# Optimization experiments

Hardware: AMD Instinct MI355X
Metric: run time of the kernel (lower is better)

The kernel has to match this reference:

```python
import jax, jax.numpy as jnp
import numpy as np
from jax import lax

COND, PRED, DH, NOUT = 64, 32, 128, 1
M, LQ, N, LR = 8, 256, 64, 512


def setup_inputs() -> dict:
    key = jax.random.key(0)
    ks = jax.random.split(key, 8)
    g = lambda k, sh, s=0.05: jax.random.normal(k, sh, jnp.float32) * s
    return {
        "query": jax.random.normal(ks[0], (M, LQ), jnp.float32),
        "ref": jax.random.normal(ks[1], (N, LR), jnp.float32),
        "q_weight": g(ks[2], (DH, 1, COND)),
        "q_bias": jnp.zeros((DH,), jnp.float32),
        "k_weight": g(ks[3], (DH, 1, COND)),
        "k_bias": jnp.zeros((DH,), jnp.float32),
        "v_weight": g(ks[4], (DH, 1, PRED), 0.1),
        "v_bias": jnp.zeros((DH,), jnp.float32),
        "m_weight": jnp.full((NOUT, 1, COND), 1.0 / COND, jnp.float32),
        "m_bias": jnp.zeros((NOUT,), jnp.float32),
        "o_weight": g(ks[5], (NOUT * PRED, DH), 0.1),
        "o_bias": jnp.zeros((NOUT * PRED,), jnp.float32),
        "m_key": g(ks[6], (1, 1, DH), 1.0),
    }


DN = ('NCH', 'OIH', 'NCH')


def _minmax_conv(x, w, b, offset=None, scale=None):
    # x: [B,1,L], w: [H,1,k] -> y: [B,H,W]. Each length-k window is min-max
    # normalized before the conv contraction. Since offset/scale are constant
    # per window: conv((x-off)/sc) = (conv(x) - off*sum(w)) / sc.
    k = w.shape[-1]
    if offset is None:
        offset = lax.reduce_window(x, jnp.inf, lax.min, (1, 1, k), (1, 1, 1), 'VALID')
    if scale is None:
        mx = lax.reduce_window(x, -jnp.inf, lax.max, (1, 1, k), (1, 1, 1), 'VALID')
        scale = mx - offset
        scale = jnp.where(scale == 0.0, 1.0, scale)
    raw = lax.conv_general_dilated(x, w, (1,), 'VALID', dimension_numbers=DN)
    wsum = w.sum(axis=(1, 2))
    y = (raw - offset * wsum[None, :, None]) / scale + b[None, :, None]
    return y, offset, scale


def reference(query, ref, q_weight, q_bias, k_weight, k_bias, v_weight, v_bias,
              m_weight, m_bias, o_weight, o_bias, m_key):
    cond, pred = q_weight.shape[-1], v_weight.shape[-1]
    # ---- query encoding ----
    q_in = jnp.cumsum(query, axis=1)[:, None, :]
    q, q_off, q_scale = _minmax_conv(q_in, q_weight, q_bias)
    q = q.transpose(0, 2, 1)                   # [M,Q,H]
    Qn = q.shape[1]
    q_scale_t = q_scale.transpose(0, 2, 1)     # [M,Q,1]
    qp = jnp.pad(query, ((0, 0), (cond - 1, 0)))[:, None, :]
    mc = lax.conv_general_dilated(qp, m_weight, (1,), 'VALID', dimension_numbers=DN)
    mc = mc + m_bias[None, :, None]
    mc = mc[..., cond - pred:]                 # [M,NOUT,Q+pred-1]
    widx = jnp.arange(pred)[:, None] + jnp.arange(Qn)[None, :]
    mwin = mc[..., widx]                       # [M,NOUT,pred,Q]
    m = mwin.reshape(mwin.shape[0], -1, Qn).transpose(0, 2, 1)  # [M,Q,NOUT*pred]
    m = m / q_scale_t
    # ---- key / value encoding ----
    k_in = jnp.cumsum(ref, axis=1)[:, None, :-pred]
    k, k_off, k_scale = _minmax_conv(k_in, k_weight, k_bias)
    k = k.transpose(0, 2, 1)                   # [N,K,H]
    v_in = ref[:, None, cond:]
    v, _, _ = _minmax_conv(v_in, v_weight, v_bias,
                           offset=jnp.zeros_like(k_off), scale=k_scale)
    v = v.transpose(0, 2, 1)                   # [N,K,H]
    # ---- scores ----
    full_score = jnp.einsum('mqh,nkh->mqkn', q, k)           # [M,Q,K,N]
    m_score = jnp.sum(q * m_key, axis=-1, keepdims=True)     # [M,Q,1]
    # ---- semi-hard attention: top-1 window per reference series ----
    ref_score = full_score.max(axis=2)         # [M,Q,N]
    max_idx = full_score.argmax(axis=2)        # [M,Q,N]
    n_ids = jnp.arange(v.shape[0])[None, None, :]
    sel_v = v[n_ids, max_idx]                  # [M,Q,N,H]
    sel_v = sel_v @ o_weight.T + o_bias        # [M,Q,N,D]
    scores = jax.nn.softmax(jnp.concatenate([ref_score, m_score], axis=-1), axis=-1)
    rs, ms = scores[..., :-1], scores[..., -1:]
    p = jnp.einsum('mqn,mqnd->mqd', rs, sel_v) + ms * m      # [M,Q,D]
    return p * q_scale_t
```

## Files before the change

kernel.cpp:

```cpp
#include <hip/hip_runtime.h>
#include <cmath>

#define M_B   8
#define LQ    256
#define N_B   64
#define LR    512
#define COND  64
#define PRED  32
#define DH    128
#define QN    193
#define KN    417
#define QPAD  256
#define KPAD  448

typedef _Float16 half8 __attribute__((ext_vector_type(8)));
typedef float f32x16 __attribute__((ext_vector_type(16)));

__device__ __forceinline__ f32x16 mfma_f16(half8 a, half8 b, f32x16 c) {
    return __builtin_amdgcn_mfma_f32_32x32x16_f16(a, b, c, 0, 0, 0);
}
__device__ __forceinline__ f32x16 zero16() {
    f32x16 z;
    #pragma unroll
    for (int i = 0; i < 16; i++) z[i] = 0.f;
    return z;
}

#define GLOAD_LDS16(g, l) __builtin_amdgcn_global_load_lds( \
    (const __attribute__((address_space(1))) void*)(g), \
    (__attribute__((address_space(3))) void*)(l), 16, 0, 0)

#define PIN_V(x) asm volatile("" : "+v"(x))

__launch_bounds__(256, 2)
__global__ void kA_feat(const float* __restrict__ query, const float* __restrict__ ref,
                        const float* __restrict__ qw, const float* __restrict__ qb,
                        const float* __restrict__ kw, const float* __restrict__ kb,
                        const float* __restrict__ vw, const float* __restrict__ vb,
                        float* __restrict__ q_scale, float* __restrict__ qfeat,
                        _Float16* __restrict__ qg,
                        _Float16* __restrict__ kg, float* __restrict__ vfeat) {
    __shared__ float x[512];
    __shared__ float s[512];
    __shared__ float wtot[4];
    __shared__ float buf[128 * 65];
    const int t = threadIdx.x;
    const int kl = t & 63;
    const int lane = t & 63, wv = t >> 6;
    const int hq = __builtin_amdgcn_readfirstlane(t >> 6);

    if (blockIdx.x < 448) {
        const int n = blockIdx.x / 7, chunk = blockIdx.x % 7;
        const float2 pr = *(const float2*)&ref[n * 512 + 2 * t];
        const float a = pr.x, b = pr.y;
        const float ls = a + b;
        float sc = ls;
        #pragma unroll
        for (int d = 1; d < 64; d <<= 1) {
            float v = __shfl_up(sc, d, 64);
            if (lane >= d) sc += v;
        }
        if (lane == 63) wtot[wv] = sc;
        x[2 * t] = a; x[2 * t + 1] = b;
        __syncthreads();
        float woff = 0.f;
        #pragma unroll
        for (int w2 = 0; w2 < 3; w2++) if (w2 < wv) woff += wtot[w2];
        const float excl = woff + sc - ls;
        s[2 * t] = excl + a;
        s[2 * t + 1] = excl + a + b;
        __syncthreads();

        const int kp = chunk * 64 + kl;
        const bool vkp = kp < KN;
        float csw[64];
        float mn = INFINITY, mx = -INFINITY;
        #pragma unroll
        for (int j = 0; j < 64; j++) {
            float v = s[kp + j];
            csw[j] = v;
            mn = fminf(mn, v);
            mx = fmaxf(mx, v);
        }
        float scv = mx - mn; if (scv == 0.f) scv = 1.f;
        const float inv = 1.f / scv;
        #pragma unroll
        for (int j = 0; j < 64; j++) { csw[j] -= mn; PIN_V(csw[j]); }

        for (int hh = 0; hh < 32; hh++) {
            const int h = hq * 32 + hh;
            const float* wrow = kw + h * 64;
            float a0 = 0.f, a1 = 0.f, a2 = 0.f, a3 = 0.f;
            #pragma unroll
            for (int j = 0; j < 64; j += 4) {
                a0 = fmaf(wrow[j],     csw[j],     a0);
                a1 = fmaf(wrow[j + 1], csw[j + 1], a1);
                a2 = fmaf(wrow[j + 2], csw[j + 2], a2);
                a3 = fmaf(wrow[j + 3], csw[j + 3], a3);
            }
            float kraw = (a0 + a1) + (a2 + a3);
            float kval = vkp ? kraw * inv + kb[h] : 0.f;
            buf[h * 65 + (kl ^ (h >> 3))] = kval;
        }
        __syncthreads();
        {
            const size_t nb = ((size_t)n * KPAD + chunk * 64) * 256;
            #pragma unroll
            for (int r = 0; r < 8; r++) {
                int task = r * 256 + t;
                int kp_l = task >> 5, g = task & 31;
                int cb = g & 15, lo = g >> 4;
                half8 hv;
                #pragma unroll
                for (int jj = 0; jj < 8; jj++) {
                    float v = buf[(cb * 8 + jj) * 65 + (kp_l ^ cb)];
                    _Float16 hi = (_Float16)v;
                    hv[jj] = lo ? (_Float16)((v - (float)hi) * 1024.0f) : hi;
                }
                *(half8*)&kg[nb + (size_t)kp_l * 256 + ((size_t)(g ^ (kp_l & 31)) << 3)] = hv;
            }
        }
        __syncthreads();
        float refw[32];
        #pragma unroll
        for (int j = 0; j < 32; j++) {
            int ri = 64 + kp + j;
            refw[j] = (ri < 512) ? x[ri] : 0.f;
            PIN_V(refw[j]);
        }
        for (int hh = 0; hh < 32; hh++) {
            const int h = hq * 32 + hh;
            const float* vrow = vw + h * 32;
            float b0 = 0.f, b1 = 0.f;
            #pragma unroll
            for (int j = 0; j < 32; j += 2) {
                b0 = fmaf(vrow[j],     refw[j],     b0);
                b1 = fmaf(vrow[j + 1], refw[j + 1], b1);
            }
            float vval = vkp ? (b0 + b1) * inv + vb[h] : 0.f;
            buf[h * 65 + (kl ^ (h >> 3))] = vval;
        }
        __syncthreads();
        {
            const size_t vb0 = ((size_t)n * KPAD + chunk * 64) * 128;
            #pragma unroll
            for (int r = 0; r < 8; r++) {
                int idx = r * 256 + t;
                int kp_l = idx >> 5, c4 = idx & 31;
                float4 o;
                o.x = buf[(c4 * 4 + 0) * 65 + (kp_l ^ ((c4 * 4 + 0) >> 3))];
                o.y = buf[(c4 * 4 + 1) * 65 + (kp_l ^ ((c4 * 4 + 1) >> 3))];
                o.z = buf[(c4 * 4 + 2) * 65 + (kp_l ^ ((c4 * 4 + 2) >> 3))];
                o.w = buf[(c4 * 4 + 3) * 65 + (kp_l ^ ((c4 * 4 + 3) >> 3))];
                *(float4*)&vfeat[vb0 + (size_t)kp_l * 128 + c4 * 4] = o;
            }
        }
    } else {
        const int id = blockIdx.x - 448;
        const int m = id >> 2, qc = id & 3;
        const float a = query[m * 256 + t];
        float sc = a;
        #pragma unroll
        for (int d = 1; d < 64; d <<= 1) {
            float v = __shfl_up(sc, d, 64);
            if (lane >= d) sc += v;
        }
        if (lane == 63) wtot[wv] = sc;
        __syncthreads();
        float woff = 0.f;
        #pragma unroll
        for (int w2 = 0; w2 < 3; w2++) if (w2 < wv) woff += wtot[w2];
        s[t] = woff + sc;
        __syncthreads();

        const int qpos = qc * 64 + kl;
        const bool vq = qpos < QN;
        const int base = vq ? qpos : (QN - 1);
        float csw[64];
        float mn = INFINITY, mx = -INFINITY;
        #pragma unroll
        for (int j = 0; j < 64; j++) {
            float v = s[base + j];
            csw[j] = v;
            mn = fminf(mn, v);
            mx = fmaxf(mx, v);
        }
        float sq = mx - mn; if (sq == 0.f) sq = 1.f;
        const float inv = 1.f / sq;
        if (t < 64) q_scale[m * QPAD + qpos] = vq ? sq : 1.f;
        #pragma unroll
        for (int j = 0; j < 64; j++) { csw[j] -= mn; PIN_V(csw[j]); }

        for (int hh = 0; hh < 32; hh++) {
            const int h = hq * 32 + hh;
            const float* wrow = qw + h * 64;
            float a0 = 0.f, a1 = 0.f, a2 = 0.f, a3 = 0.f;
            #pragma unroll
            for (int j = 0; j < 64; j += 4) {
                a0 = fmaf(wrow[j],     csw[j],     a0);
                a1 = fmaf(wrow[j + 1], csw[j + 1], a1);
                a2 = fmaf(wrow[j + 2], csw[j + 2], a2);
                a3 = fmaf(wrow[j + 3], csw[j + 3], a3);
            }
            float raw = (a0 + a1) + (a2 + a3);
            float val = vq ? raw * inv + qb[h] : 0.f;
            buf[h * 65 + (kl ^ (h >> 3))] = val;
        }
        __syncthreads();
        const size_t qb0 = ((size_t)m * QPAD + qc * 64) * 128;
        #pragma unroll
        for (int r = 0; r < 8; r++) {
            int idx = r * 256 + t;
            int qp_l = idx >> 5, c4 = idx & 31;
            float4 o;
            o.x = buf[(c4 * 4 + 0) * 65 + (qp_l ^ ((c4 * 4 + 0) >> 3))];
            o.y = buf[(c4 * 4 + 1) * 65 + (qp_l ^ ((c4 * 4 + 1) >> 3))];
            o.z = buf[(c4 * 4 + 2) * 65 + (qp_l ^ ((c4 * 4 + 2) >> 3))];
            o.w = buf[(c4 * 4 + 3) * 65 + (qp_l ^ ((c4 * 4 + 3) >> 3))];
            *(float4*)&qfeat[qb0 + (size_t)qp_l * 128 + c4 * 4] = o;
        }
        #pragma unroll
        for (int r = 0; r < 8; r++) {
            int idx = r * 256 + t;
            int qp_l = idx >> 5, g = idx & 31;
            int c = g >> 2, kh = (g >> 1) & 1, lo = g & 1;
            half8 hv;
            #pragma unroll
            for (int jj = 0; jj < 8; jj++) {
                int h = c * 16 + kh * 8 + jj;
                float v = buf[h * 65 + (qp_l ^ (h >> 3))];
                _Float16 hi = (_Float16)v;
                hv[jj] = lo ? (_Float16)((v - (float)hi) * 1024.0f) : hi;
            }
            int qp2 = qc * 64 + qp_l;
            int grp = (m << 3) | (qp2 >> 5);
            size_t fb = (size_t)(grp * 16 + c * 2 + lo);
            *(half8*)&qg[fb * 512 + (size_t)(kh * 32 + (qp2 & 31)) * 8] = hv;
        }
    }
}

__launch_bounds__(256, 2)
__global__ void k3_score(const _Float16* __restrict__ qg, const _Float16* __restrict__ kg,
                         float* __restrict__ bscore, int* __restrict__ bidx) {
    __shared__ _Float16 Kbuf[4][32 * 256];
    const int blk = blockIdx.x;
    const int n = blk & 63, qt = blk >> 6;
    const int t = threadIdx.x, w = t >> 6, l = t & 63;
    const int lrow = l & 31, khalf = l >> 5;

    half8 qf[2][8][2];
    #pragma unroll
    for (int r = 0; r < 2; r++) {
        const int grp = (qt * 4 + w) * 2 + r;
        #pragma unroll
        for (int c = 0; c < 8; c++)
            #pragma unroll
            for (int h = 0; h < 2; h++)
                qf[r][c][h] = ((const half8*)qg)[(size_t)(grp * 16 + c * 2 + h) * 64 + l];
    }

    const _Float16* ksrc = kg + (size_t)n * KPAD * 256;

    float best[2][16];
    unsigned bkt[4] = {0u, 0u, 0u, 0u};
    #pragma unroll
    for (int r = 0; r < 2; r++)
        #pragma unroll
        for (int g = 0; g < 16; g++) best[r][g] = -INFINITY;

    #pragma unroll
    for (int rd = 0; rd < 4; rd++) {
        int e = (rd * 4 + w) * 512 + l * 8;
        GLOAD_LDS16(ksrc + e, &Kbuf[0][0] + e);
    }
    #pragma unroll
    for (int rd = 0; rd < 4; rd++) {
        int e = (rd * 4 + w) * 512 + l * 8;
        GLOAD_LDS16(ksrc + 32 * 256 + e, &Kbuf[1][0] + e);
    }

    for (int kt = 0; kt < 14; kt++) {
        if (kt < 12) {
            const _Float16* src = ksrc + (size_t)(kt + 2) * (32 * 256);
            _Float16* dst = &Kbuf[(kt + 2) & 3][0];
            #pragma unroll
            for (int rd = 0; rd < 4; rd++) {
                int e = (rd * 4 + w) * 512 + l * 8;
                GLOAD_LDS16(src + e, dst + e);
            }
            asm volatile("s_waitcnt vmcnt(8)" ::: "memory");
        } else if (kt == 12) {
            asm volatile("s_waitcnt vmcnt(4)" ::: "memory");
        } else {
            asm volatile("s_waitcnt vmcnt(0)" ::: "memory");
        }
        asm volatile("s_barrier" ::: "memory");

        const _Float16* kb = &Kbuf[kt & 3][0];
        f32x16 accH[2], accL[2];
        accH[0] = zero16(); accH[1] = zero16();
        accL[0] = zero16(); accL[1] = zero16();
        #pragma unroll
        for (int c = 0; c < 8; c++) {
            half8 bh = *(const half8*)(kb + lrow * 256 + (((c * 2 + khalf) ^ lrow) * 8));
            half8 bl = *(const half8*)(kb + lrow * 256 + (((16 + c * 2 + khalf) ^ lrow) * 8));
            #pragma unroll
            for (int r = 0; r < 2; r++) {
                accH[r] = mfma_f16(qf[r][c][0], bh, accH[r]);
                accL[r] = mfma_f16(qf[r][c][0], bl, accL[r]);
                accL[r] = mfma_f16(qf[r][c][1], bh, accL[r]);
            }
        }
        const int kp = kt * 32 + lrow;
        const bool valid = kp < KN;
        #pragma unroll
        for (int r = 0; r < 2; r++) {
            #pragma unroll
            for (int g = 0; g < 16; g++) {
                float sv = fmaf(accL[r][g], 0.0009765625f, accH[r][g]);
                if (valid && (sv > best[r][g])) {
                    best[r][g] = sv;
                    const int slot = r * 16 + g;
                    const unsigned sh = (unsigned)(slot & 7) * 4u;
                    bkt[slot >> 3] = (bkt[slot >> 3] & ~(0xFu << sh)) | ((unsigned)kt << sh);
                }
            }
        }
    }

    #pragma unroll
    for (int r = 0; r < 2; r++) {
        #pragma unroll
        for (int g = 0; g < 16; g++) {
            float sv = best[r][g];
            const int slot = r * 16 + g;
            int ktb = (int)((bkt[slot >> 3] >> ((slot & 7) * 4)) & 0xFu);
            int kp = ktb * 32 + lrow;
            for (int msk = 1; msk < 32; msk <<= 1) {
                float os = __shfl_xor(sv, msk, 64);
                int okp = __shfl_xor(kp, msk, 64);
                if (os > sv || (os == sv && okp < kp)) { sv = os; kp = okp; }
            }
            if (lrow == 0) {
                int row = (g & 3) + 8 * (g >> 2) + 4 * khalf;
                int mq = (qt * 4 + w) * 64 + r * 32 + row;
                if ((mq & 255) < QN) {
                    bscore[(size_t)mq * 64 + n] = sv;
                    bidx[(size_t)mq * 64 + n] = kp;
                }
            }
        }
    }
}

__global__ void k4_out(const float* __restrict__ query,
                       const float* __restrict__ qfeat, const float* __restrict__ vfeat,
                       const float* __restrict__ bscore, const int* __restrict__ bidx,
                       const float* __restrict__ q_scale,
                       const float* __restrict__ mw, const float* __restrict__ mb,
                       const float* __restrict__ mkey,
                       const float* __restrict__ ow, const float* __restrict__ ob,
                       float* __restrict__ out) {
    __shared__ float rsS[4][64];
    __shared__ int   idxS[4][64];
    __shared__ float wS[4][128];
    const int t = threadIdx.x, wv = t >> 6, l = t & 63;
    const int j = blockIdx.x * 4 + wv;
    const int m = j / QN, qpos = j - m * QN;
    const int mq = m * QPAD + qpos;

    float s = bscore[(size_t)mq * 64 + l];
    int idx = bidx[(size_t)mq * 64 + l];
    float msv = qfeat[(size_t)mq * 128 + l] * mkey[l]
              + qfeat[(size_t)mq * 128 + 64 + l] * mkey[64 + l];
    #pragma unroll
    for (int msk = 1; msk < 64; msk <<= 1) msv += __shfl_xor(msv, msk, 64);
    float mx = s;
    #pragma unroll
    for (int msk = 1; msk < 64; msk <<= 1) mx = fmaxf(mx, __shfl_xor(mx, msk, 64));
    mx = fmaxf(mx, msv);
    float e = expf(s - mx);
    float sum = e;
    #pragma unroll
    for (int msk = 1; msk < 64; msk <<= 1) sum += __shfl_xor(sum, msk, 64);
    float ems = expf(msv - mx);
    float inv = 1.f / (sum + ems);
    float rs = e * inv, msw = ems * inv;

    rsS[wv][l] = rs; idxS[wv][l] = idx;
    __syncthreads();
    float ax = 0.f, ay = 0.f;
    #pragma unroll 8
    for (int nn = 0; nn < 64; nn++) {
        float r = rsS[wv][nn];
        int id = idxS[wv][nn];
        const float2 v = *(const float2*)&vfeat[((size_t)nn * KPAD + id) * 128 + 2 * l];
        ax = fmaf(r, v.x, ax);
        ay = fmaf(r, v.y, ay);
    }
    wS[wv][2 * l] = ax; wS[wv][2 * l + 1] = ay;
    __syncthreads();
    if (l < 32) {
        float p = 0.f;
        #pragma unroll
        for (int h4 = 0; h4 < 32; h4++) {
            const float4 wv4 = *(const float4*)&wS[wv][h4 * 4];
            const float4 o4 = *(const float4*)&ow[l * 128 + h4 * 4];
            p += wv4.x * o4.x + wv4.y * o4.y + wv4.z * o4.z + wv4.w * o4.w;
        }
        p += (1.f - msw) * ob[l];
        float mcv = mb[0];
        const int tpos = 32 + qpos + l;
        for (int jj = 0; jj < 64; jj++) {
            int qi = tpos + jj - 63;
            if (qi >= 0) mcv = fmaf(mw[jj], query[m * 256 + qi], mcv);
        }
        float outv = q_scale[mq] * p + msw * mcv;
        out[(size_t)j * 32 + l] = outv;
    }
}

extern "C" void kernel_launch(void* const* d_in, const int* in_sizes, int n_in,
                              void* d_out, int out_size, void* d_ws, size_t ws_size,
                              hipStream_t stream) {
    const float* query = (const float*)d_in[0];
    const float* ref   = (const float*)d_in[1];
    const float* qw    = (const float*)d_in[2];
    const float* qb    = (const float*)d_in[3];
    const float* kw    = (const float*)d_in[4];
    const float* kb    = (const float*)d_in[5];
    const float* vw    = (const float*)d_in[6];
    const float* vb    = (const float*)d_in[7];
    const float* mw    = (const float*)d_in[8];
    const float* mb    = (const float*)d_in[9];
    const float* ow    = (const float*)d_in[10];
    const float* ob    = (const float*)d_in[11];
    const float* mkey  = (const float*)d_in[12];
    float* out = (float*)d_out;

    float* ws = (float*)d_ws;
    float* q_scale = ws;
    float* qfeat   = ws + 2048;
    float* bscore  = ws + 264192;
    int*   bidx    = (int*)(ws + 395264);
    _Float16* qg   = (_Float16*)(ws + 526336);
    _Float16* kg   = (_Float16*)(ws + 788480);
    float* vfeat   = ws + 4458496;

    hipLaunchKernelGGL(kA_feat, dim3(480), dim3(256), 0, stream,
                       query, ref, qw, qb, kw, kb, vw, vb,
                       q_scale, qfeat, qg, kg, vfeat);
    hipLaunchKernelGGL(k3_score, dim3(512), dim3(256), 0, stream,
                       qg, kg, bscore, bidx);
    hipLaunchKernelGGL(k4_out, dim3(386), dim3(256), 0, stream,
                       query, qfeat, vfeat, bscore, bidx, q_scale, mw, mb, mkey, ow, ob, out);
}
```

Measured before the change: 200.3 us.

## Split score kernel's key range across two blocks and merge argmax in output kernel

The score kernel now splits the 14 key tiles per reference series into two halves, each handled by its own block, which doubles the grid from 512 to 1024 blocks. Each half writes its own best score and index, and the output kernel merges the pair with a vector load and a compare. The aim is to fill more compute units and shorten each block's serial loop. LDS use drops from four buffers to two, so the prefetch pipeline becomes shallower, with a block-wide barrier every iteration. The q fragments are also loaded twice and the intermediate buffers grow, with workspace offsets shifted to fit.

```diff
diff --git a/kernel.cpp b/kernel.cpp
--- a/kernel.cpp
+++ b/kernel.cpp
@@ -243,9 +243,9 @@
 __launch_bounds__(256, 2)
 __global__ void k3_score(const _Float16* __restrict__ qg, const _Float16* __restrict__ kg,
                          float* __restrict__ bscore, int* __restrict__ bidx) {
-    __shared__ _Float16 Kbuf[4][32 * 256];
+    __shared__ _Float16 Kbuf[2][32 * 256];
     const int blk = blockIdx.x;
-    const int n = blk & 63, qt = blk >> 6;
+    const int n = blk & 63, qt = (blk >> 6) & 7, half = blk >> 9;
     const int t = threadIdx.x, w = t >> 6, l = t & 63;
     const int lrow = l & 31, khalf = l >> 5;
 
@@ -260,7 +260,7 @@
                 qf[r][c][h] = ((const half8*)qg)[(size_t)(grp * 16 + c * 2 + h) * 64 + l];
     }
 
-    const _Float16* ksrc = kg + (size_t)n * KPAD * 256;
+    const _Float16* ksrc = kg + (size_t)n * KPAD * 256 + (size_t)half * 7 * (32 * 256);
 
     float best[2][16];
     unsigned bkt[4] = {0u, 0u, 0u, 0u};
@@ -274,30 +274,19 @@
         int e = (rd * 4 + w) * 512 + l * 8;
         GLOAD_LDS16(ksrc + e, &Kbuf[0][0] + e);
     }
-    #pragma unroll
-    for (int rd = 0; rd < 4; rd++) {
-        int e = (rd * 4 + w) * 512 + l * 8;
-        GLOAD_LDS16(ksrc + 32 * 256 + e, &Kbuf[1][0] + e);
-    }
-
-    for (int kt = 0; kt < 14; kt++) {
-        if (kt < 12) {
-            const _Float16* src = ksrc + (size_t)(kt + 2) * (32 * 256);
-            _Float16* dst = &Kbuf[(kt + 2) & 3][0];
+
+    for (int kt = 0; kt < 7; kt++) {
+        __syncthreads();
+        if (kt < 6) {
+            const _Float16* src = ksrc + (size_t)(kt + 1) * (32 * 256);
+            _Float16* dst = &Kbuf[(kt + 1) & 1][0];
             #pragma unroll
             for (int rd = 0; rd < 4; rd++) {
                 int e = (rd * 4 + w) * 512 + l * 8;
                 GLOAD_LDS16(src + e, dst + e);
             }
-            asm volatile("s_waitcnt vmcnt(8)" ::: "memory");
-        } else if (kt == 12) {
-            asm volatile("s_waitcnt vmcnt(4)" ::: "memory");
-        } else {
-            asm volatile("s_waitcnt vmcnt(0)" ::: "memory");
-        }
-        asm volatile("s_barrier" ::: "memory");
-
-        const _Float16* kb = &Kbuf[kt & 3][0];
+        }
+        const _Float16* kb = &Kbuf[kt & 1][0];
         f32x16 accH[2], accL[2];
         accH[0] = zero16(); accH[1] = zero16();
         accL[0] = zero16(); accL[1] = zero16();
@@ -312,7 +301,8 @@
                 accL[r] = mfma_f16(qf[r][c][1], bh, accL[r]);
             }
         }
-        const int kp = kt * 32 + lrow;
+        const int sub = half * 7 + kt;
+        const int kp = sub * 32 + lrow;
         const bool valid = kp < KN;
         #pragma unroll
         for (int r = 0; r < 2; r++) {
@@ -323,7 +313,7 @@
                     best[r][g] = sv;
                     const int slot = r * 16 + g;
                     const unsigned sh = (unsigned)(slot & 7) * 4u;
-                    bkt[slot >> 3] = (bkt[slot >> 3] & ~(0xFu << sh)) | ((unsigned)kt << sh);
+                    bkt[slot >> 3] = (bkt[slot >> 3] & ~(0xFu << sh)) | ((unsigned)sub << sh);
                 }
             }
         }
@@ -335,8 +325,8 @@
         for (int g = 0; g < 16; g++) {
             float sv = best[r][g];
             const int slot = r * 16 + g;
-            int ktb = (int)((bkt[slot >> 3] >> ((slot & 7) * 4)) & 0xFu);
-            int kp = ktb * 32 + lrow;
+            int sub = (int)((bkt[slot >> 3] >> ((slot & 7) * 4)) & 0xFu);
+            int kp = sub * 32 + lrow;
             for (int msk = 1; msk < 32; msk <<= 1) {
                 float os = __shfl_xor(sv, msk, 64);
                 int okp = __shfl_xor(kp, msk, 64);
@@ -346,8 +336,8 @@
                 int row = (g & 3) + 8 * (g >> 2) + 4 * khalf;
                 int mq = (qt * 4 + w) * 64 + r * 32 + row;
                 if ((mq & 255) < QN) {
-                    bscore[(size_t)mq * 64 + n] = sv;
-                    bidx[(size_t)mq * 64 + n] = kp;
+                    bscore[(((size_t)mq * 64 + n) << 1) + half] = sv;
+                    bidx[(((size_t)mq * 64 + n) << 1) + half] = kp;
                 }
             }
         }
@@ -370,8 +360,11 @@
     const int m = j / QN, qpos = j - m * QN;
     const int mq = m * QPAD + qpos;
 
-    float s = bscore[(size_t)mq * 64 + l];
-    int idx = bidx[(size_t)mq * 64 + l];
+    const float2 s2 = *(const float2*)&bscore[((size_t)mq * 64 + l) << 1];
+    const int2  i2 = *(const int2*)&bidx[((size_t)mq * 64 + l) << 1];
+    float s = s2.x; int idx = i2.x;
+    if (s2.y > s) { s = s2.y; idx = i2.y; }
+
     float msv = qfeat[(size_t)mq * 128 + l] * mkey[l]
               + qfeat[(size_t)mq * 128 + 64 + l] * mkey[64 + l];
     #pragma unroll
@@ -443,15 +436,15 @@
     float* q_scale = ws;
     float* qfeat   = ws + 2048;
     float* bscore  = ws + 264192;
-    int*   bidx    = (int*)(ws + 395264);
-    _Float16* qg   = (_Float16*)(ws + 526336);
-    _Float16* kg   = (_Float16*)(ws + 788480);
-    float* vfeat   = ws + 4458496;
+    int*   bidx    = (int*)(ws + 526336);
+    _Float16* qg   = (_Float16*)(ws + 788480);
+    _Float16* kg   = (_Float16*)(ws + 1050624);
+    float* vfeat   = ws + 4720640;
 
     hipLaunchKernelGGL(kA_feat, dim3(480), dim3(256), 0, stream,
                        query, ref, qw, qb, kw, kb, vw, vb,
                        q_scale, qfeat, qg, kg, vfeat);
-    hipLaunchKernelGGL(k3_score, dim3(512), dim3(256), 0, stream,
+    hipLaunchKernelGGL(k3_score, dim3(1024), dim3(256), 0, stream,
                        qg, kg, bscore, bidx);
     hipLaunchKernelGGL(k4_out, dim3(386), dim3(256), 0, stream,
                        query, qfeat, vfeat, bscore, bidx, q_scale, mw, mb, mkey, ow, ob, out);
```

After: 214.4 us. 7.0% more time.
